# Kernel tuning notes

Measured on AMD Instinct MI355X. Metric: run time of the kernel, lower is better.

## Reference

```python
import jax, jax.numpy as jnp
import numpy as np

D_MODEL, WIN, STRIDE, NHEAD, HEAD_DIM, FFN_H = 96, 16, 8, 6, 16, 192
INNER = NHEAD * HEAD_DIM
EPS = 1e-5


def _ln(x, g, b):
    m = jnp.mean(x, axis=-1, keepdims=True)
    v = jnp.mean((x - m) ** 2, axis=-1, keepdims=True)
    return (x - m) / jnp.sqrt(v + EPS) * g + b


def setup_inputs() -> dict:
    key = jax.random.key(0)
    ks = jax.random.split(key, 16)
    B, L, D = 32, 8192, D_MODEL
    sd = lambda n: 1.0 / np.sqrt(n)
    return {
        "x": jax.random.normal(ks[0], (B, L, D), jnp.float32),
        "ln1_g": jnp.ones((D,), jnp.float32),
        "ln1_b": jnp.zeros((D,), jnp.float32),
        "qkv_w": jax.random.normal(ks[1], (D, 3 * INNER), jnp.float32) * sd(D),
        "qkv_b": jnp.zeros((3 * INNER,), jnp.float32),
        "out_w": jax.random.normal(ks[2], (INNER, D), jnp.float32) * sd(INNER),
        "out_b": jnp.zeros((D,), jnp.float32),
        "ln2_g": jnp.ones((D,), jnp.float32),
        "ln2_b": jnp.zeros((D,), jnp.float32),
        "ffn_w1": jax.random.normal(ks[3], (D, FFN_H), jnp.float32) * sd(D),
        "ffn_b1": jnp.zeros((FFN_H,), jnp.float32),
        "ffn_w2": jax.random.normal(ks[4], (FFN_H, D), jnp.float32) * sd(FFN_H),
        "ffn_b2": jnp.zeros((D,), jnp.float32),
        "pln_g": jnp.ones((D,), jnp.float32),
        "pln_b": jnp.zeros((D,), jnp.float32),
    }


def reference(x, ln1_g, ln1_b, qkv_w, qkv_b, out_w, out_b,
              ln2_g, ln2_b, ffn_w1, ffn_b1, ffn_w2, ffn_b2, pln_g, pln_b):
    B, L, D = x.shape
    w, s = WIN, STRIDE
    num_win = 1 + (L - w) // s  # all windows fit since (num_win-1)*s + w <= L
    idx = jnp.arange(num_win)[:, None] * s + jnp.arange(w)[None, :]  # [N, w]

    seg = x[:, idx]  # [B, N, w, D] gather of overlapping windows

    # --- pre-LN attention block, vectorized over all windows ---
    h = _ln(seg, ln1_g, ln1_b)
    qkv = h @ qkv_w + qkv_b  # [B, N, w, 3*INNER]
    q, k, v = jnp.split(qkv, 3, axis=-1)
    shp = (B, num_win, w, NHEAD, HEAD_DIM)
    q, k, v = q.reshape(shp), k.reshape(shp), v.reshape(shp)
    scores = jnp.einsum('bnqhd,bnkhd->bnhqk', q, k) / np.sqrt(HEAD_DIM).astype(np.float32)
    causal = jnp.tril(jnp.ones((w, w), bool))
    scores = jnp.where(causal, scores, -jnp.inf)
    attn = jax.nn.softmax(scores, axis=-1)
    o = jnp.einsum('bnhqk,bnkhd->bnqhd', attn, v).reshape(B, num_win, w, INNER)
    o = o @ out_w + out_b
    h = seg + o

    # --- FFN block ---
    h2 = _ln(h, ln2_g, ln2_b)
    h = h + (jax.nn.gelu(h2 @ ffn_w1 + ffn_b1) @ ffn_w2 + ffn_b2)
    h = _ln(h, pln_g, pln_b)

    # --- overlap-add average ---
    out = jnp.zeros((B, L, D), x.dtype).at[:, idx].add(h)
    cnt = jnp.zeros((L,), x.dtype).at[idx.reshape(-1)].add(1.0)
    return out / jnp.maximum(cnt, 1.0)[None, :, None]
```

## Files before the change

kernel.cpp:

```cpp
#include <hip/hip_runtime.h>
#include <hip/hip_bf16.h>

typedef __attribute__((ext_vector_type(8))) short short8;
typedef __attribute__((ext_vector_type(4))) float f32x4;
typedef __attribute__((ext_vector_type(4))) unsigned u32x4;

#define LDS_BYTES 40960
#define SH   104
#define SU   52
#define KOFF 3328
#define VOFF 6656
#define F1S  200
#define F1SU 100

#if __has_builtin(__builtin_amdgcn_cvt_pk_bf16_f32)
typedef __attribute__((ext_vector_type(2))) __bf16 bf16x2;
__device__ __forceinline__ unsigned pk2bf(float a, float b){
  bf16x2 v = __builtin_amdgcn_cvt_pk_bf16_f32(a, b);
  return __builtin_bit_cast(unsigned, v);
}
__device__ __forceinline__ unsigned short f2bf(float x){
  bf16x2 v = __builtin_amdgcn_cvt_pk_bf16_f32(x, x);
  return (unsigned short)(__builtin_bit_cast(unsigned, v) & 0xFFFFu);
}
#else
__device__ __forceinline__ unsigned short f2bf(float x){
  unsigned u = __float_as_uint(x);
  u += 0x7FFFu + ((u >> 16) & 1u);
  return (unsigned short)(u >> 16);
}
__device__ __forceinline__ unsigned pk2bf(float a, float b){
  return (unsigned)f2bf(a) | ((unsigned)f2bf(b) << 16);
}
#endif

#if __has_builtin(__builtin_amdgcn_rcpf)
__device__ __forceinline__ float fast_rcp(float x){ return __builtin_amdgcn_rcpf(x); }
#else
__device__ __forceinline__ float fast_rcp(float x){ return 1.f/x; }
#endif
#if __has_builtin(__builtin_amdgcn_rsqf)
__device__ __forceinline__ float fast_rsq(float x){ return __builtin_amdgcn_rsqf(x); }
#else
__device__ __forceinline__ float fast_rsq(float x){ return rsqrtf(x); }
#endif

__device__ __forceinline__ float bflo(unsigned u){ return __uint_as_float(u << 16); }
__device__ __forceinline__ float bfhi(unsigned u){ return __uint_as_float(u & 0xFFFF0000u); }
__device__ __forceinline__ float bf1(unsigned short h){ return __uint_as_float(((unsigned)h) << 16); }

__global__ void zero_stripes(float* __restrict__ out){
  int k = blockIdx.x;
  int b = blockIdx.y;
  int t = threadIdx.x;
  int tok = 24*k + (t / 24);
  f32x4 z = {0.f, 0.f, 0.f, 0.f};
  *(f32x4*)(out + ((size_t)b*8192 + tok)*96 + 4*(t % 24)) = z;
}

__global__ void pack_weights(const float* __restrict__ qkv_w, const float* __restrict__ out_w,
                             const float* __restrict__ ffn_w1, const float* __restrict__ ffn_w2,
                             short8* __restrict__ wsv){
  int f = blockIdx.x, lane = threadIdx.x;
  const float* W; int N, nt, kf;
  if (f < 54)      { W = qkv_w;  N = 288; nt = f/3;        kf = f%3; }
  else if (f < 72) { int i=f-54;  W = out_w;  N = 96;  nt = i/3; kf = i%3; }
  else if (f < 108){ int i=f-72;  W = ffn_w1; N = 192; nt = i/3; kf = i%3; }
  else             { int i=f-108; W = ffn_w2; N = 96;  nt = i/6; kf = i%6; }
  int n = lane & 15, kq = lane >> 4;
  short8 v;
#pragma unroll
  for (int j = 0; j < 8; ++j){
    int k = kf*32 + kq*8 + j;
    v[j] = (short)f2bf(W[(size_t)k * N + nt*16 + n]);
  }
  wsv[f*64 + lane] = v;
}

__global__ __launch_bounds__(512, 8)
void fused_block(const float* __restrict__ x,
                 const float* __restrict__ ln1_g, const float* __restrict__ ln1_b,
                 const float* __restrict__ qkv_b,
                 const float* __restrict__ out_b,
                 const float* __restrict__ ln2_g, const float* __restrict__ ln2_b,
                 const float* __restrict__ ffn_b1, const float* __restrict__ ffn_b2,
                 const float* __restrict__ pln_g, const float* __restrict__ pln_b,
                 const short8* __restrict__ wsv,
                 float* __restrict__ out)
{
  __shared__ __align__(16) char smem[LDS_BYTES];
  unsigned short* hres  = (unsigned short*)smem;
  unsigned*       hresU = (unsigned*)smem;
  unsigned short* buf1  = (unsigned short*)(smem + 9984);
  unsigned*       buf1U = (unsigned*)(smem + 9984);
  unsigned short* buf2  = (unsigned short*)(smem + 19968);
  unsigned*       buf2U = (unsigned*)(smem + 19968);

  const int tid  = threadIdx.x;
  const int wave = tid >> 6, lane = tid & 63;
  const int lm   = lane & 15, quad = lane >> 4;
  __builtin_assume(wave >= 0 && wave < 8);
  __builtin_assume(lm >= 0 && lm < 16);
  __builtin_assume(quad >= 0 && quad < 4);
  const int g = blockIdx.x, b = blockIdx.y;
  const int t0 = 24 * g;
  const size_t xbase = ((size_t)b * 8192 + t0) * 96;
  const short8* wl = wsv + lane;

  {
    const int row = tid >> 4, j = tid & 15;
    const float* xr = x + xbase + (size_t)row*96 + 6*j;
    float v[6];
#pragma unroll
    for (int e = 0; e < 3; ++e){ float2 t = *(const float2*)(xr + 2*e); v[2*e]=t.x; v[2*e+1]=t.y; }
    float s = 0.f, q2 = 0.f;
#pragma unroll
    for (int e = 0; e < 6; ++e){ s += v[e]; q2 += v[e]*v[e]; }
#pragma unroll
    for (int m = 1; m < 16; m <<= 1){ s += __shfl_xor(s, m, 16); q2 += __shfl_xor(q2, m, 16); }
    float mean = s * (1.f/96.f);
    float rstd = fast_rsq(q2 * (1.f/96.f) - mean*mean + 1e-5f);
#pragma unroll
    for (int e = 0; e < 3; ++e){
      float2 gg = *(const float2*)(ln1_g + 6*j + 2*e);
      float2 bb = *(const float2*)(ln1_b + 6*j + 2*e);
      buf1U[row*SU + 3*j + e] = pk2bf((v[2*e]-mean)*rstd*gg.x+bb.x,
                                      (v[2*e+1]-mean)*rstd*gg.y+bb.y);
    }
  }
  __syncthreads();

  {
    const int mt = wave & 1, p = wave >> 1;
    __builtin_assume(p >= 0 && p < 4);
    const unsigned short* arow = buf1 + (16*mt + lm)*SH + quad*8;
    short8 h0 = *(const short8*)(arow);
    short8 h1 = *(const short8*)(arow + 32);
    short8 h2 = *(const short8*)(arow + 64);
    auto qkv_tile = [&](int nt){
      if (nt < 12){
        f32x4 acc = *(const f32x4*)(qkv_b + nt*16 + quad*4);
        acc = __builtin_amdgcn_mfma_f32_16x16x32_bf16(wl[(nt*3+0)*64], h0, acc, 0, 0, 0);
        acc = __builtin_amdgcn_mfma_f32_16x16x32_bf16(wl[(nt*3+1)*64], h1, acc, 0, 0, 0);
        acc = __builtin_amdgcn_mfma_f32_16x16x32_bf16(wl[(nt*3+2)*64], h2, acc, 0, 0, 0);
        int row = 16*mt + lm;
        unsigned idx = (nt < 6)
          ? (unsigned)(row*SU + nt*8 + quad*2)
          : (unsigned)((KOFF>>1) + row*SU + (nt-6)*8 + quad*2);
        buf2U[idx]     = pk2bf(acc[0], acc[1]);
        buf2U[idx + 1] = pk2bf(acc[2], acc[3]);
      } else {
        int col = nt*16 + lm;
        float bias = qkv_b[col];
        f32x4 acc = {bias, bias, bias, bias};
        acc = __builtin_amdgcn_mfma_f32_16x16x32_bf16(h0, wl[(nt*3+0)*64], acc, 0, 0, 0);
        acc = __builtin_amdgcn_mfma_f32_16x16x32_bf16(h1, wl[(nt*3+1)*64], acc, 0, 0, 0);
        acc = __builtin_amdgcn_mfma_f32_16x16x32_bf16(h2, wl[(nt*3+2)*64], acc, 0, 0, 0);
        int d2 = col - 192;
        int w0 = (VOFF >> 1) + d2*20 + 8*mt + 2*quad;
        buf2U[w0]     = pk2bf(acc[0], acc[1]);
        buf2U[w0 + 1] = pk2bf(acc[2], acc[3]);
      }
    };
#pragma unroll
    for (int i = 0; i < 4; ++i) qkv_tile(p + 4*i);
    if (p < 2) qkv_tile(p + 16);
  }
  __syncthreads();

  {
    auto attn_unit = [&](int u){
      int w = u / 6, h = u - 6*(u / 6);
      short8 qa = {0,0,0,0,0,0,0,0}, ka = {0,0,0,0,0,0,0,0};
      if (quad < 2){
        qa = *(const short8*)(buf2 +        (8*w + lm)*SH + h*16 + quad*8);
        ka = *(const short8*)(buf2 + KOFF + (8*w + lm)*SH + h*16 + quad*8);
      }
      f32x4 sc = {0.f,0.f,0.f,0.f};
      sc = __builtin_amdgcn_mfma_f32_16x16x32_bf16(ka, qa, sc, 0, 0, 0);
      float p4[4]; float sum = 0.f;
#pragma unroll
      for (int r = 0; r < 4; ++r){
        int k = quad*4 + r;
        float e = __expf(sc[r]*0.25f);
        p4[r] = (k <= lm) ? e : 0.f;
        sum += p4[r];
      }
      sum += __shfl_xor(sum, 16);
      sum += __shfl_xor(sum, 32);
      float rs = fast_rcp(sum);
      int x0 = (int)pk2bf(p4[0]*rs, p4[1]*rs);
      int x1 = (int)pk2bf(p4[2]*rs, p4[3]*rs);
      int srcA = lm + ((quad & 1) << 5);
      int e0 = __shfl(x0, srcA),      e1 = __shfl(x1, srcA);
      int e2 = __shfl(x0, srcA + 16), e3 = __shfl(x1, srcA + 16);
      short8 pa = {0,0,0,0,0,0,0,0}, va = {0,0,0,0,0,0,0,0};
      if (quad < 2){
        u32x4 t = {(unsigned)e0, (unsigned)e1, (unsigned)e2, (unsigned)e3};
        pa = __builtin_bit_cast(short8, t);
        va = *(const short8*)(buf2 + VOFF + (h*16 + lm)*40 + 8*w + quad*8);
      }
      f32x4 oc = {0.f,0.f,0.f,0.f};
      oc = __builtin_amdgcn_mfma_f32_16x16x32_bf16(va, pa, oc, 0, 0, 0);
      unsigned ob = (w*16 + lm)*SU + h*8 + quad*2;
      buf1U[ob]     = pk2bf(oc[0], oc[1]);
      buf1U[ob + 1] = pk2bf(oc[2], oc[3]);
    };
    attn_unit(wave);
    attn_unit(wave + 8);
    if (wave < 2) attn_unit(wave + 16);
  }
  __syncthreads();

  {
    auto oproj_tile = [&](int tile){
      int w = tile / 6, nt = tile - 6*(tile / 6);
      f32x4 acc = *(const f32x4*)(out_b + nt*16 + quad*4);
#pragma unroll
      for (int kf = 0; kf < 3; ++kf){
        short8 bfr = *(const short8*)(buf1 + (w*16 + lm)*SH + kf*32 + quad*8);
        acc = __builtin_amdgcn_mfma_f32_16x16x32_bf16(wl[(54 + nt*3 + kf)*64], bfr, acc, 0, 0, 0);
      }
      f32x4 xr = *(const f32x4*)(x + xbase + (size_t)(8*w + lm)*96 + nt*16 + quad*4);
      unsigned idx = (w*16 + lm)*SU + nt*8 + quad*2;
      hresU[idx]     = pk2bf(acc[0]+xr[0], acc[1]+xr[1]);
      hresU[idx + 1] = pk2bf(acc[2]+xr[2], acc[3]+xr[3]);
    };
    oproj_tile(wave);
    oproj_tile(wave + 8);
    if (wave < 2) oproj_tile(wave + 16);
  }
  __syncthreads();

  {
    const int j = tid & 15;
#pragma unroll
    for (int p = 0; p < 2; ++p){
      int row = p*32 + (tid >> 4);
      if (row < 48){
        float v[6];
#pragma unroll
        for (int e = 0; e < 3; ++e){
          unsigned u = hresU[row*SU + 3*j + e];
          v[2*e] = bflo(u); v[2*e+1] = bfhi(u);
        }
        float s = 0.f, q2 = 0.f;
#pragma unroll
        for (int e = 0; e < 6; ++e){ s += v[e]; q2 += v[e]*v[e]; }
#pragma unroll
        for (int m = 1; m < 16; m <<= 1){ s += __shfl_xor(s, m, 16); q2 += __shfl_xor(q2, m, 16); }
        float mean = s * (1.f/96.f);
        float rstd = fast_rsq(q2 * (1.f/96.f) - mean*mean + 1e-5f);
#pragma unroll
        for (int e = 0; e < 3; ++e){
          float2 gg = *(const float2*)(ln2_g + 6*j + 2*e);
          float2 bb = *(const float2*)(ln2_b + 6*j + 2*e);
          buf1U[row*SU + 3*j + e] = pk2bf((v[2*e]-mean)*rstd*gg.x+bb.x,
                                          (v[2*e+1]-mean)*rstd*gg.y+bb.y);
        }
      }
    }
  }
  __syncthreads();

  {
    auto ffn1_tile = [&](int tile){
      int mt = tile % 3, nt = tile / 3;
      f32x4 acc = *(const f32x4*)(ffn_b1 + nt*16 + quad*4);
#pragma unroll
      for (int kf = 0; kf < 3; ++kf){
        short8 bfr = *(const short8*)(buf1 + (mt*16 + lm)*SH + kf*32 + quad*8);
        acc = __builtin_amdgcn_mfma_f32_16x16x32_bf16(wl[(72 + nt*3 + kf)*64], bfr, acc, 0, 0, 0);
      }
      float gl[4];
#pragma unroll
      for (int r = 0; r < 4; ++r){
        float uu = acc[r];
        float z2n = -1.5957691216f * (uu + 0.044715f * uu*uu*uu);
        float e = __expf(z2n);
        gl[r] = uu * fast_rcp(1.f + e);
      }
      unsigned idx = (mt*16 + lm)*F1SU + nt*8 + quad*2;
      buf2U[idx]     = pk2bf(gl[0], gl[1]);
      buf2U[idx + 1] = pk2bf(gl[2], gl[3]);
    };
#pragma unroll
    for (int i = 0; i < 4; ++i) ffn1_tile(wave + 8*i);
    if (wave < 4) ffn1_tile(wave + 32);
  }
  __syncthreads();

  {
    auto ffn2_tile = [&](int tile){
      int mt = tile / 6, nt = tile - 6*(tile / 6);
      f32x4 acc = *(const f32x4*)(ffn_b2 + nt*16 + quad*4);
#pragma unroll
      for (int kf = 0; kf < 6; ++kf){
        short8 bfr = *(const short8*)(buf2 + (mt*16 + lm)*F1S + kf*32 + quad*8);
        acc = __builtin_amdgcn_mfma_f32_16x16x32_bf16(wl[(108 + nt*6 + kf)*64], bfr, acc, 0, 0, 0);
      }
      unsigned idx = (mt*16 + lm)*SU + nt*8 + quad*2;
      unsigned u0 = hresU[idx], u1 = hresU[idx + 1];
      hresU[idx]     = pk2bf(bflo(u0)+acc[0], bfhi(u0)+acc[1]);
      hresU[idx + 1] = pk2bf(bflo(u1)+acc[2], bfhi(u1)+acc[3]);
    };
    ffn2_tile(wave);
    ffn2_tile(wave + 8);
    if (wave < 2) ffn2_tile(wave + 16);
  }
  __syncthreads();

  {
    const int i = tid >> 4, c0 = tid & 15;
    const int l = t0 + i;
    const size_t obase = ((size_t)b * 8192 + l) * 96;
    int rowA, rowB = -1;
    if (i < 8)       rowA = i;
    else if (i < 16){ rowA = i;            rowB = 16 + (i - 8); }
    else if (i < 24){ rowA = 16 + (i - 8); rowB = 32 + (i - 16); }
    else             rowA = 32 + (i - 16);

    float g6[6], b6[6];
#pragma unroll
    for (int e = 0; e < 6; ++e){ g6[e] = pln_g[c0 + 16*e]; b6[e] = pln_b[c0 + 16*e]; }

    float yA[6];
    {
      float v[6];
#pragma unroll
      for (int e = 0; e < 6; ++e) v[e] = bf1(hres[rowA*SH + c0 + 16*e]);
      float s = 0.f, q2 = 0.f;
#pragma unroll
      for (int e = 0; e < 6; ++e){ s += v[e]; q2 += v[e]*v[e]; }
#pragma unroll
      for (int m = 1; m < 16; m <<= 1){ s += __shfl_xor(s, m, 16); q2 += __shfl_xor(q2, m, 16); }
      float mean = s * (1.f/96.f);
      float rstd = fast_rsq(q2 * (1.f/96.f) - mean*mean + 1e-5f);
#pragma unroll
      for (int e = 0; e < 6; ++e) yA[e] = (v[e]-mean)*rstd*g6[e] + b6[e];
    }
    if (rowB >= 0){
      float yB[6];
      {
        float v[6];
#pragma unroll
        for (int e = 0; e < 6; ++e) v[e] = bf1(hres[rowB*SH + c0 + 16*e]);
        float s = 0.f, q2 = 0.f;
#pragma unroll
        for (int e = 0; e < 6; ++e){ s += v[e]; q2 += v[e]*v[e]; }
#pragma unroll
        for (int m = 1; m < 16; m <<= 1){ s += __shfl_xor(s, m, 16); q2 += __shfl_xor(q2, m, 16); }
        float mean = s * (1.f/96.f);
        float rstd = fast_rsq(q2 * (1.f/96.f) - mean*mean + 1e-5f);
#pragma unroll
        for (int e = 0; e < 6; ++e) yB[e] = (v[e]-mean)*rstd*g6[e] + b6[e];
      }
#pragma unroll
      for (int e = 0; e < 6; ++e)
        out[obase + c0 + 16*e] = 0.5f * (yA[e] + yB[e]);
    } else {
      float inv = (l < 8 || l >= 8184) ? 1.0f : 0.5f;
#pragma unroll
      for (int e = 0; e < 6; ++e)
        atomicAdd(&out[obase + c0 + 16*e], yA[e] * inv);
    }
  }
}

extern "C" void kernel_launch(void* const* d_in, const int* in_sizes, int n_in,
                              void* d_out, int out_size, void* d_ws, size_t ws_size,
                              hipStream_t stream) {
  const float* x      = (const float*)d_in[0];
  const float* ln1_g  = (const float*)d_in[1];
  const float* ln1_b  = (const float*)d_in[2];
  const float* qkv_w  = (const float*)d_in[3];
  const float* qkv_b  = (const float*)d_in[4];
  const float* out_w  = (const float*)d_in[5];
  const float* out_b  = (const float*)d_in[6];
  const float* ln2_g  = (const float*)d_in[7];
  const float* ln2_b  = (const float*)d_in[8];
  const float* ffn_w1 = (const float*)d_in[9];
  const float* ffn_b1 = (const float*)d_in[10];
  const float* ffn_w2 = (const float*)d_in[11];
  const float* ffn_b2 = (const float*)d_in[12];
  const float* pln_g  = (const float*)d_in[13];
  const float* pln_b  = (const float*)d_in[14];
  float* out = (float*)d_out;
  short8* wsv = (short8*)d_ws;

  zero_stripes<<<dim3(342, 32), 192, 0, stream>>>(out);
  pack_weights<<<144, 64, 0, stream>>>(qkv_w, out_w, ffn_w1, ffn_w2, wsv);
  fused_block<<<dim3(341, 32), 512, 0, stream>>>(
      x, ln1_g, ln1_b, qkv_b, out_b, ln2_g, ln2_b, ffn_b1, ffn_b2,
      pln_g, pln_b, (const short8*)wsv, out);
}
```

Baseline: 419.9 us.

## Reuse A-fragments across N tiles, split MFMA accumulators, hoist attention loads

The out-projection, FFN1 and FFN2 stages are reassigned so that 6 waves each load their A-row fragments once and reuse them across several N tiles, replacing the old scheme of 8 waves each reloading fragments per tile. MFMA chains are split across two accumulators to shorten the dependency chain. The Q/K/V fragment loads for all attention units are hoisted ahead of the compute, and exp is replaced by exp2 with prescaled constants. This cuts LDS traffic and MFMA latency stalls, but leaves 2 of the 8 waves idle in those stages and raises register pressure.

```diff
diff --git a/kernel.cpp b/kernel.cpp
--- a/kernel.cpp
+++ b/kernel.cpp
@@ -43,6 +43,11 @@
 __device__ __forceinline__ float fast_rsq(float x){ return __builtin_amdgcn_rsqf(x); }
 #else
 __device__ __forceinline__ float fast_rsq(float x){ return rsqrtf(x); }
+#endif
+#if __has_builtin(__builtin_amdgcn_exp2f)
+__device__ __forceinline__ float fast_ex2(float x){ return __builtin_amdgcn_exp2f(x); }
+#else
+__device__ __forceinline__ float fast_ex2(float x){ return exp2f(x); }
 #endif
 
 __device__ __forceinline__ float bflo(unsigned u){ return __uint_as_float(u << 16); }
@@ -139,27 +144,29 @@
     short8 h2 = *(const short8*)(arow + 64);
     auto qkv_tile = [&](int nt){
       if (nt < 12){
-        f32x4 acc = *(const f32x4*)(qkv_b + nt*16 + quad*4);
-        acc = __builtin_amdgcn_mfma_f32_16x16x32_bf16(wl[(nt*3+0)*64], h0, acc, 0, 0, 0);
-        acc = __builtin_amdgcn_mfma_f32_16x16x32_bf16(wl[(nt*3+1)*64], h1, acc, 0, 0, 0);
-        acc = __builtin_amdgcn_mfma_f32_16x16x32_bf16(wl[(nt*3+2)*64], h2, acc, 0, 0, 0);
+        f32x4 acc0 = *(const f32x4*)(qkv_b + nt*16 + quad*4);
+        f32x4 acc1 = {0.f,0.f,0.f,0.f};
+        acc0 = __builtin_amdgcn_mfma_f32_16x16x32_bf16(wl[(nt*3+0)*64], h0, acc0, 0, 0, 0);
+        acc1 = __builtin_amdgcn_mfma_f32_16x16x32_bf16(wl[(nt*3+1)*64], h1, acc1, 0, 0, 0);
+        acc0 = __builtin_amdgcn_mfma_f32_16x16x32_bf16(wl[(nt*3+2)*64], h2, acc0, 0, 0, 0);
         int row = 16*mt + lm;
         unsigned idx = (nt < 6)
           ? (unsigned)(row*SU + nt*8 + quad*2)
           : (unsigned)((KOFF>>1) + row*SU + (nt-6)*8 + quad*2);
-        buf2U[idx]     = pk2bf(acc[0], acc[1]);
-        buf2U[idx + 1] = pk2bf(acc[2], acc[3]);
+        buf2U[idx]     = pk2bf(acc0[0]+acc1[0], acc0[1]+acc1[1]);
+        buf2U[idx + 1] = pk2bf(acc0[2]+acc1[2], acc0[3]+acc1[3]);
       } else {
         int col = nt*16 + lm;
         float bias = qkv_b[col];
-        f32x4 acc = {bias, bias, bias, bias};
-        acc = __builtin_amdgcn_mfma_f32_16x16x32_bf16(h0, wl[(nt*3+0)*64], acc, 0, 0, 0);
-        acc = __builtin_amdgcn_mfma_f32_16x16x32_bf16(h1, wl[(nt*3+1)*64], acc, 0, 0, 0);
-        acc = __builtin_amdgcn_mfma_f32_16x16x32_bf16(h2, wl[(nt*3+2)*64], acc, 0, 0, 0);
+        f32x4 acc0 = {bias, bias, bias, bias};
+        f32x4 acc1 = {0.f,0.f,0.f,0.f};
+        acc0 = __builtin_amdgcn_mfma_f32_16x16x32_bf16(h0, wl[(nt*3+0)*64], acc0, 0, 0, 0);
+        acc1 = __builtin_amdgcn_mfma_f32_16x16x32_bf16(h1, wl[(nt*3+1)*64], acc1, 0, 0, 0);
+        acc0 = __builtin_amdgcn_mfma_f32_16x16x32_bf16(h2, wl[(nt*3+2)*64], acc0, 0, 0, 0);
         int d2 = col - 192;
         int w0 = (VOFF >> 1) + d2*20 + 8*mt + 2*quad;
-        buf2U[w0]     = pk2bf(acc[0], acc[1]);
-        buf2U[w0 + 1] = pk2bf(acc[2], acc[3]);
+        buf2U[w0]     = pk2bf(acc0[0]+acc1[0], acc0[1]+acc1[1]);
+        buf2U[w0 + 1] = pk2bf(acc0[2]+acc1[2], acc0[3]+acc1[3]);
       }
     };
 #pragma unroll
@@ -169,20 +176,32 @@
   __syncthreads();
 
   {
-    auto attn_unit = [&](int u){
-      int w = u / 6, h = u - 6*(u / 6);
-      short8 qa = {0,0,0,0,0,0,0,0}, ka = {0,0,0,0,0,0,0,0};
-      if (quad < 2){
-        qa = *(const short8*)(buf2 +        (8*w + lm)*SH + h*16 + quad*8);
-        ka = *(const short8*)(buf2 + KOFF + (8*w + lm)*SH + h*16 + quad*8);
-      }
+    const short8 z8 = {0,0,0,0,0,0,0,0};
+    short8 qa0=z8,ka0=z8,va0=z8, qa1=z8,ka1=z8,va1=z8, qa2=z8,ka2=z8,va2=z8;
+    const int u0 = wave, u1 = wave + 8, u2 = wave + 16;
+    const int w0_=u0/6, h0_=u0-6*(u0/6), w1_=u1/6, h1_=u1-6*(u1/6);
+    const int w2_=u2/6, h2_=u2-6*(u2/6);
+    if (quad < 2){
+      qa0 = *(const short8*)(buf2 +        (8*w0_ + lm)*SH + h0_*16 + quad*8);
+      ka0 = *(const short8*)(buf2 + KOFF + (8*w0_ + lm)*SH + h0_*16 + quad*8);
+      va0 = *(const short8*)(buf2 + VOFF + (h0_*16 + lm)*40 + 8*w0_ + quad*8);
+      qa1 = *(const short8*)(buf2 +        (8*w1_ + lm)*SH + h1_*16 + quad*8);
+      ka1 = *(const short8*)(buf2 + KOFF + (8*w1_ + lm)*SH + h1_*16 + quad*8);
+      va1 = *(const short8*)(buf2 + VOFF + (h1_*16 + lm)*40 + 8*w1_ + quad*8);
+      if (wave < 2){
+        qa2 = *(const short8*)(buf2 +        (8*w2_ + lm)*SH + h2_*16 + quad*8);
+        ka2 = *(const short8*)(buf2 + KOFF + (8*w2_ + lm)*SH + h2_*16 + quad*8);
+        va2 = *(const short8*)(buf2 + VOFF + (h2_*16 + lm)*40 + 8*w2_ + quad*8);
+      }
+    }
+    auto attn_compute = [&](short8 qa, short8 ka, short8 va, int w, int h){
       f32x4 sc = {0.f,0.f,0.f,0.f};
       sc = __builtin_amdgcn_mfma_f32_16x16x32_bf16(ka, qa, sc, 0, 0, 0);
       float p4[4]; float sum = 0.f;
 #pragma unroll
       for (int r = 0; r < 4; ++r){
         int k = quad*4 + r;
-        float e = __expf(sc[r]*0.25f);
+        float e = fast_ex2(sc[r]*0.36067376f);
         p4[r] = (k <= lm) ? e : 0.f;
         sum += p4[r];
       }
@@ -194,11 +213,10 @@
       int srcA = lm + ((quad & 1) << 5);
       int e0 = __shfl(x0, srcA),      e1 = __shfl(x1, srcA);
       int e2 = __shfl(x0, srcA + 16), e3 = __shfl(x1, srcA + 16);
-      short8 pa = {0,0,0,0,0,0,0,0}, va = {0,0,0,0,0,0,0,0};
+      short8 pa = z8;
       if (quad < 2){
         u32x4 t = {(unsigned)e0, (unsigned)e1, (unsigned)e2, (unsigned)e3};
         pa = __builtin_bit_cast(short8, t);
-        va = *(const short8*)(buf2 + VOFF + (h*16 + lm)*40 + 8*w + quad*8);
       }
       f32x4 oc = {0.f,0.f,0.f,0.f};
       oc = __builtin_amdgcn_mfma_f32_16x16x32_bf16(va, pa, oc, 0, 0, 0);
@@ -206,29 +224,34 @@
       buf1U[ob]     = pk2bf(oc[0], oc[1]);
       buf1U[ob + 1] = pk2bf(oc[2], oc[3]);
     };
-    attn_unit(wave);
-    attn_unit(wave + 8);
-    if (wave < 2) attn_unit(wave + 16);
-  }
-  __syncthreads();
-
-  {
-    auto oproj_tile = [&](int tile){
-      int w = tile / 6, nt = tile - 6*(tile / 6);
-      f32x4 acc = *(const f32x4*)(out_b + nt*16 + quad*4);
-#pragma unroll
-      for (int kf = 0; kf < 3; ++kf){
-        short8 bfr = *(const short8*)(buf1 + (w*16 + lm)*SH + kf*32 + quad*8);
-        acc = __builtin_amdgcn_mfma_f32_16x16x32_bf16(wl[(54 + nt*3 + kf)*64], bfr, acc, 0, 0, 0);
-      }
-      f32x4 xr = *(const f32x4*)(x + xbase + (size_t)(8*w + lm)*96 + nt*16 + quad*4);
+    attn_compute(qa0, ka0, va0, w0_, h0_);
+    attn_compute(qa1, ka1, va1, w1_, h1_);
+    if (wave < 2) attn_compute(qa2, ka2, va2, w2_, h2_);
+  }
+  __syncthreads();
+
+  if (wave < 6){
+    const int w = wave >> 1, ntb = (wave & 1)*3;
+    const unsigned short* arow = buf1 + (w*16 + lm)*SH + quad*8;
+    short8 a0 = *(const short8*)(arow);
+    short8 a1 = *(const short8*)(arow + 32);
+    short8 a2 = *(const short8*)(arow + 64);
+    f32x4 xr[3];
+#pragma unroll
+    for (int i = 0; i < 3; ++i)
+      xr[i] = *(const f32x4*)(x + xbase + (size_t)(8*w + lm)*96 + (ntb+i)*16 + quad*4);
+#pragma unroll
+    for (int i = 0; i < 3; ++i){
+      int nt = ntb + i;
+      f32x4 acc0 = *(const f32x4*)(out_b + nt*16 + quad*4);
+      f32x4 acc1 = {0.f,0.f,0.f,0.f};
+      acc0 = __builtin_amdgcn_mfma_f32_16x16x32_bf16(wl[(54 + nt*3 + 0)*64], a0, acc0, 0, 0, 0);
+      acc1 = __builtin_amdgcn_mfma_f32_16x16x32_bf16(wl[(54 + nt*3 + 1)*64], a1, acc1, 0, 0, 0);
+      acc0 = __builtin_amdgcn_mfma_f32_16x16x32_bf16(wl[(54 + nt*3 + 2)*64], a2, acc0, 0, 0, 0);
       unsigned idx = (w*16 + lm)*SU + nt*8 + quad*2;
-      hresU[idx]     = pk2bf(acc[0]+xr[0], acc[1]+xr[1]);
-      hresU[idx + 1] = pk2bf(acc[2]+xr[2], acc[3]+xr[3]);
-    };
-    oproj_tile(wave);
-    oproj_tile(wave + 8);
-    if (wave < 2) oproj_tile(wave + 16);
+      hresU[idx]     = pk2bf(acc0[0]+acc1[0]+xr[i][0], acc0[1]+acc1[1]+xr[i][1]);
+      hresU[idx + 1] = pk2bf(acc0[2]+acc1[2]+xr[i][2], acc0[3]+acc1[3]+xr[i][3]);
+    }
   }
   __syncthreads();
 
@@ -263,50 +286,60 @@
   }
   __syncthreads();
 
-  {
-    auto ffn1_tile = [&](int tile){
-      int mt = tile % 3, nt = tile / 3;
-      f32x4 acc = *(const f32x4*)(ffn_b1 + nt*16 + quad*4);
-#pragma unroll
-      for (int kf = 0; kf < 3; ++kf){
-        short8 bfr = *(const short8*)(buf1 + (mt*16 + lm)*SH + kf*32 + quad*8);
-        acc = __builtin_amdgcn_mfma_f32_16x16x32_bf16(wl[(72 + nt*3 + kf)*64], bfr, acc, 0, 0, 0);
-      }
+  if (wave < 6){
+    const int mt = wave >> 1, ntb = (wave & 1)*6;
+    const unsigned short* arow = buf1 + (mt*16 + lm)*SH + quad*8;
+    short8 a0 = *(const short8*)(arow);
+    short8 a1 = *(const short8*)(arow + 32);
+    short8 a2 = *(const short8*)(arow + 64);
+#pragma unroll
+    for (int i = 0; i < 6; ++i){
+      int nt = ntb + i;
+      f32x4 acc0 = *(const f32x4*)(ffn_b1 + nt*16 + quad*4);
+      f32x4 acc1 = {0.f,0.f,0.f,0.f};
+      acc0 = __builtin_amdgcn_mfma_f32_16x16x32_bf16(wl[(72 + nt*3 + 0)*64], a0, acc0, 0, 0, 0);
+      acc1 = __builtin_amdgcn_mfma_f32_16x16x32_bf16(wl[(72 + nt*3 + 1)*64], a1, acc1, 0, 0, 0);
+      acc0 = __builtin_amdgcn_mfma_f32_16x16x32_bf16(wl[(72 + nt*3 + 2)*64], a2, acc0, 0, 0, 0);
       float gl[4];
 #pragma unroll
       for (int r = 0; r < 4; ++r){
-        float uu = acc[r];
-        float z2n = -1.5957691216f * (uu + 0.044715f * uu*uu*uu);
-        float e = __expf(z2n);
+        float uu = acc0[r] + acc1[r];
+        float z = -2.3022081f * (uu + 0.044715f * uu*uu*uu);
+        float e = fast_ex2(z);
         gl[r] = uu * fast_rcp(1.f + e);
       }
       unsigned idx = (mt*16 + lm)*F1SU + nt*8 + quad*2;
       buf2U[idx]     = pk2bf(gl[0], gl[1]);
       buf2U[idx + 1] = pk2bf(gl[2], gl[3]);
-    };
-#pragma unroll
-    for (int i = 0; i < 4; ++i) ffn1_tile(wave + 8*i);
-    if (wave < 4) ffn1_tile(wave + 32);
-  }
-  __syncthreads();
-
-  {
-    auto ffn2_tile = [&](int tile){
-      int mt = tile / 6, nt = tile - 6*(tile / 6);
-      f32x4 acc = *(const f32x4*)(ffn_b2 + nt*16 + quad*4);
-#pragma unroll
-      for (int kf = 0; kf < 6; ++kf){
-        short8 bfr = *(const short8*)(buf2 + (mt*16 + lm)*F1S + kf*32 + quad*8);
-        acc = __builtin_amdgcn_mfma_f32_16x16x32_bf16(wl[(108 + nt*6 + kf)*64], bfr, acc, 0, 0, 0);
-      }
+    }
+  }
+  __syncthreads();
+
+  if (wave < 6){
+    const int mt = wave >> 1, ntb = (wave & 1)*3;
+    const unsigned short* frow = buf2 + (mt*16 + lm)*F1S + quad*8;
+    short8 f0 = *(const short8*)(frow);
+    short8 f1 = *(const short8*)(frow + 32);
+    short8 f2 = *(const short8*)(frow + 64);
+    short8 f3 = *(const short8*)(frow + 96);
+    short8 f4 = *(const short8*)(frow + 128);
+    short8 f5 = *(const short8*)(frow + 160);
+#pragma unroll
+    for (int i = 0; i < 3; ++i){
+      int nt = ntb + i;
+      f32x4 acc0 = *(const f32x4*)(ffn_b2 + nt*16 + quad*4);
+      f32x4 acc1 = {0.f,0.f,0.f,0.f};
+      acc0 = __builtin_amdgcn_mfma_f32_16x16x32_bf16(wl[(108 + nt*6 + 0)*64], f0, acc0, 0, 0, 0);
+      acc1 = __builtin_amdgcn_mfma_f32_16x16x32_bf16(wl[(108 + nt*6 + 1)*64], f1, acc1, 0, 0, 0);
+      acc0 = __builtin_amdgcn_mfma_f32_16x16x32_bf16(wl[(108 + nt*6 + 2)*64], f2, acc0, 0, 0, 0);
+      acc1 = __builtin_amdgcn_mfma_f32_16x16x32_bf16(wl[(108 + nt*6 + 3)*64], f3, acc1, 0, 0, 0);
+      acc0 = __builtin_amdgcn_mfma_f32_16x16x32_bf16(wl[(108 + nt*6 + 4)*64], f4, acc0, 0, 0, 0);
+      acc1 = __builtin_amdgcn_mfma_f32_16x16x32_bf16(wl[(108 + nt*6 + 5)*64], f5, acc1, 0, 0, 0);
       unsigned idx = (mt*16 + lm)*SU + nt*8 + quad*2;
       unsigned u0 = hresU[idx], u1 = hresU[idx + 1];
-      hresU[idx]     = pk2bf(bflo(u0)+acc[0], bfhi(u0)+acc[1]);
-      hresU[idx + 1] = pk2bf(bflo(u1)+acc[2], bfhi(u1)+acc[3]);
-    };
-    ffn2_tile(wave);
-    ffn2_tile(wave + 8);
-    if (wave < 2) ffn2_tile(wave + 16);
+      hresU[idx]     = pk2bf(bflo(u0)+acc0[0]+acc1[0], bfhi(u0)+acc0[1]+acc1[1]);
+      hresU[idx + 1] = pk2bf(bflo(u1)+acc0[2]+acc1[2], bfhi(u1)+acc0[3]+acc1[3]);
+    }
   }
   __syncthreads();
 
```

After: 449.6 us. +7.1%, slower.
